# Kernel optimization log

Hardware: AMD Instinct MI355X
Metric: run time of the kernel (lower is better)

Reference implementation:

```python
import jax, jax.numpy as jnp
import numpy as np

# CODABlocks (codomain attention) with per_channel_attention=True:
# token_codimension = head_codimension = 1, scale = 2, n_modes = [32, 32],
# mixer_modes = [16, 16], temperature = 1.0, instance_norm (affine) everywhere.
N_HEADS = 16
TEMPERATURE = 1.0
EPS = 1e-5

def _gelu(z):
    return jax.nn.gelu(z, approximate=False)  # matches torch F.gelu default (erf)

def instance_norm(x, g, b):
    # x: (B, C, H, W); normalize over spatial dims per (sample, channel), affine.
    mu = jnp.mean(x, axis=(-2, -1), keepdims=True)
    var = jnp.var(x, axis=(-2, -1), keepdims=True)
    return (x - mu) * jax.lax.rsqrt(var + EPS) * g[:, None, None] + b[:, None, None]

def conv1x1(x, w, b):
    return jnp.einsum('bihw,io->bohw', x, w) + b[None, :, None, None]

def fourier_resample(x, out_shape):
    # FFT-based spatial resampling (mode truncation / zero-pad), norm='forward'.
    if tuple(x.shape[-2:]) == tuple(out_shape):
        return x
    Ho, Wo = out_shape
    xft = jnp.fft.rfftn(x, axes=(-2, -1), norm='forward')
    out = jnp.zeros(x.shape[:-2] + (Ho, Wo // 2 + 1), dtype=xft.dtype)
    hk = min(x.shape[-2], Ho) // 2
    wk = min(xft.shape[-1], Wo // 2 + 1)
    out = out.at[..., :hk, :wk].set(xft[..., :hk, :wk])
    out = out.at[..., -hk:, :wk].set(xft[..., -hk:, :wk])
    return jnp.fft.irfftn(out, s=out_shape, axes=(-2, -1), norm='forward')

def spectral_conv(x, w, out_shape):
    # Truncated-mode spectral convolution (dense weights, equiv. to tucker rank=1.0).
    # w: (Cin, Cout, 2*mh, mw, 2) -> complex weight on kept Fourier modes.
    wc = w[..., 0] + 1j * w[..., 1]
    mh = wc.shape[2] // 2
    mw = wc.shape[3]
    Ho, Wo = out_shape
    xft = jnp.fft.rfftn(x, axes=(-2, -1), norm='forward')   # (B, Cin, H, W//2+1)
    top = jnp.einsum('bihw,iohw->bohw', xft[:, :, :mh, :mw], wc[:, :, :mh])
    bot = jnp.einsum('bihw,iohw->bohw', xft[:, :, -mh:, :mw], wc[:, :, mh:])
    out_ft = jnp.zeros((x.shape[0], wc.shape[1], Ho, Wo // 2 + 1), dtype=xft.dtype)
    out_ft = out_ft.at[:, :, :mh, :mw].set(top)
    out_ft = out_ft.at[:, :, -mh:, :mw].set(bot)
    return jnp.fft.irfftn(out_ft, s=out_shape, axes=(-2, -1), norm='forward')

def fno_layer(x, spec_w, skip_w, skip_b, out_shape, norm=None, act=None):
    # One FNOBlocks layer: spectral conv + (resampled) linear skip, optional norm/act.
    xs = fourier_resample(conv1x1(x, skip_w, skip_b), out_shape)
    xf = spectral_conv(x, spec_w, out_shape)
    if norm is not None:
        xf = instance_norm(xf, *norm)
    y = xf + xs
    return act(y) if act is not None else y

def codano_forward(x, key_w, key_skip_w, key_skip_b, query_w, query_skip_w, query_skip_b, value_w, value_skip_w, value_skip_b, proj_w, proj_skip_w, proj_skip_b, norm1_g, norm1_b, attn_norm_g, attn_norm_b, norm2_g, norm2_b, mixer_w1, mixer_skip_w1, mixer_skip_b1, mixer_norm_g1, mixer_norm_b1, mixer_w2, mixer_skip_w2, mixer_skip_b2, mixer_norm_g2, mixer_norm_b2, mixer_out_g, mixer_out_b):
    b, t, H, W = x.shape   # token codim d = 1 -> channel dim == number of tokens
    tokens = x.reshape(b * t, 1, H, W)
    tokens_norm = instance_norm(tokens, norm1_g, norm1_b)
    Hs, Ws = H // 2, W // 2   # K, Q downsampled by scale = 2
    k = fno_layer(tokens_norm, key_w, key_skip_w, key_skip_b, (Hs, Ws))
    q = fno_layer(tokens_norm, query_w, query_skip_w, query_skip_b, (Hs, Ws))
    v = fno_layer(tokens_norm, value_w, value_skip_w, value_skip_b, (H, W))

    def heads_flat(z):
        hh, ww = z.shape[-2:]
        # (b*t, n_heads*d, h, w) -> (b, heads, t, d*h*w), d = 1
        return z.reshape(b, t, N_HEADS, hh * ww).transpose(0, 2, 1, 3)

    kf, qf, vf = heads_flat(k), heads_flat(q), heads_flat(v)
    scale = jnp.sqrt(jnp.asarray(kf.shape[-1], jnp.float32)) * TEMPERATURE
    dprod = jax.nn.softmax(jnp.einsum('bhtd,bhsd->bhts', qf, kf) / scale, axis=-1)
    attn = jnp.einsum('bhts,bhsd->bhtd', dprod, vf)      # (b, heads, t, H*W)
    attn = attn.transpose(0, 2, 1, 3).reshape(b * t, N_HEADS, H, W)
    # multi-head projection back to token codimension (n_heads -> 1)
    attn = fno_layer(attn, proj_w, proj_skip_w, proj_skip_b, (H, W))
    attn = instance_norm(attn + tokens, attn_norm_g, attn_norm_b)
    # permutation-equivariant mixer: 2 FNO layers shared across all tokens
    m = instance_norm(attn, norm2_g, norm2_b)
    m = fno_layer(m, mixer_w1, mixer_skip_w1, mixer_skip_b1, (H, W), norm=(mixer_norm_g1, mixer_norm_b1), act=_gelu)
    m = fno_layer(m, mixer_w2, mixer_skip_w2, mixer_skip_b2, (H, W), norm=(mixer_norm_g2, mixer_norm_b2))
    out = instance_norm(m, mixer_out_g, mixer_out_b) + attn
    return out.reshape(b, t, H, W)

def setup_inputs():
    key = jax.random.key(0)
    ks = list(jax.random.split(key, 32))
    f32 = jnp.float32
    def W_(k, shape, s=0.02):
        return (s * jax.random.normal(k, shape)).astype(f32)
    B, T, H, Wd = 4, 32, 128, 128
    mh_s, mw_s = 16, 9    # mixer_modes [16,16]: 2*(16//2) rows, 16//2+1 rfft cols
    mh_f, mw_f = 32, 17   # n_modes [32,32]
    return {
        'x': jax.random.normal(ks[0], (B, T, H, Wd), dtype=f32),
        'key_w': W_(ks[1], (1, N_HEADS, mh_s, mw_s, 2)),
        'key_skip_w': W_(ks[2], (1, N_HEADS), 0.5),
        'key_skip_b': W_(ks[3], (N_HEADS,)),
        'query_w': W_(ks[4], (1, N_HEADS, mh_s, mw_s, 2)),
        'query_skip_w': W_(ks[5], (1, N_HEADS), 0.5),
        'query_skip_b': W_(ks[6], (N_HEADS,)),
        'value_w': W_(ks[7], (1, N_HEADS, mh_s, mw_s, 2)),
        'value_skip_w': W_(ks[8], (1, N_HEADS), 0.5),
        'value_skip_b': W_(ks[9], (N_HEADS,)),
        'proj_w': W_(ks[10], (N_HEADS, 1, mh_f, mw_f, 2)),
        'proj_skip_w': W_(ks[11], (N_HEADS, 1), 0.25),
        'proj_skip_b': W_(ks[12], (1,)),
        'norm1_g': jnp.ones((1,), f32), 'norm1_b': jnp.zeros((1,), f32),
        'attn_norm_g': jnp.ones((1,), f32), 'attn_norm_b': jnp.zeros((1,), f32),
        'norm2_g': jnp.ones((1,), f32), 'norm2_b': jnp.zeros((1,), f32),
        'mixer_w1': W_(ks[13], (1, 1, mh_f, mw_f, 2)),
        'mixer_skip_w1': W_(ks[14], (1, 1), 0.5),
        'mixer_skip_b1': W_(ks[15], (1,)),
        'mixer_norm_g1': jnp.ones((1,), f32), 'mixer_norm_b1': jnp.zeros((1,), f32),
        'mixer_w2': W_(ks[16], (1, 1, mh_f, mw_f, 2)),
        'mixer_skip_w2': W_(ks[17], (1, 1), 0.5),
        'mixer_skip_b2': W_(ks[18], (1,)),
        'mixer_norm_g2': jnp.ones((1,), f32), 'mixer_norm_b2': jnp.zeros((1,), f32),
        'mixer_out_g': jnp.ones((1,), f32), 'mixer_out_b': jnp.zeros((1,), f32),
    }

def reference(x, key_w, key_skip_w, key_skip_b, query_w, query_skip_w, query_skip_b, value_w, value_skip_w, value_skip_b, proj_w, proj_skip_w, proj_skip_b, norm1_g, norm1_b, attn_norm_g, attn_norm_b, norm2_g, norm2_b, mixer_w1, mixer_skip_w1, mixer_skip_b1, mixer_norm_g1, mixer_norm_b1, mixer_w2, mixer_skip_w2, mixer_skip_b2, mixer_norm_g2, mixer_norm_b2, mixer_out_g, mixer_out_b):
    return codano_forward(x, key_w, key_skip_w, key_skip_b, query_w, query_skip_w, query_skip_b, value_w, value_skip_w, value_skip_b, proj_w, proj_skip_w, proj_skip_b, norm1_g, norm1_b, attn_norm_g, attn_norm_b, norm2_g, norm2_b, mixer_w1, mixer_skip_w1, mixer_skip_b1, mixer_norm_g1, mixer_norm_b1, mixer_w2, mixer_skip_w2, mixer_skip_b2, mixer_norm_g2, mixer_norm_b2, mixer_out_g, mixer_out_b)
```

## Files before the change

### kernel.cpp

```cpp
#include <hip/hip_runtime.h>
#include <cmath>

#define PI_F 3.14159265358979323846f
#define NTOK 128
#define NPIX 16384
#define NHEADS 16

__device__ __forceinline__ void block_reduce2(float& a, float& b){
  __shared__ float sa[4], sb[4];
  __syncthreads();
  for (int o=32;o>0;o>>=1){ a += __shfl_down(a,o); b += __shfl_down(b,o); }
  int w = threadIdx.x>>6, l = threadIdx.x&63;
  if (l==0){ sa[w]=a; sb[w]=b; }
  __syncthreads();
  a = sa[0]+sa[1]+sa[2]+sa[3];
  b = sb[0]+sb[1]+sb[2]+sb[3];
}

__device__ __forceinline__ float block_reduce1(float a){
  __shared__ float sa[4];
  __syncthreads();
  for (int o=32;o>0;o>>=1) a += __shfl_down(a,o);
  int w = threadIdx.x>>6, l = threadIdx.x&63;
  if (l==0) sa[w]=a;
  __syncthreads();
  return sa[0]+sa[1]+sa[2]+sa[3];
}

__device__ __forceinline__ float br1k(float a, float* scr){
  __syncthreads();
  for (int o=32;o>0;o>>=1) a += __shfl_down(a,o);
  int w=threadIdx.x>>6, l=threadIdx.x&63;
  if (l==0) scr[w]=a;
  __syncthreads();
  if (threadIdx.x<64){
    float v=(threadIdx.x<16)? scr[threadIdx.x] : 0.f;
    for (int o=8;o>0;o>>=1) v += __shfl_down(v,o);
    if (threadIdx.x==0) scr[16]=v;
  }
  __syncthreads();
  return scr[16];
}

__device__ __forceinline__ float gelu_f(float y){
  return 0.5f*y*(1.f + erff(y*0.70710678118f));
}

__device__ __forceinline__ void affine_from(const float* __restrict__ ps, float g, float bb, int t,
                                            float& a, float& b0){
  float sum=0.f,sq=0.f;
  #pragma unroll
  for (int s=0;s<8;s++){ const float* p=ps+((size_t)t*8+s)*2; sum+=p[0]; sq+=p[1]; }
  const float iN=1.f/NPIX;
  float mu=sum*iN, var=sq*iN-mu*mu;
  a=rsqrtf(var+1e-5f)*g;
  b0=bb-mu*a;
}
__device__ __forceinline__ void scalA_from(const float* __restrict__ psA, float ag, float n2g, int t,
                                           float& muZ, float& aA, float& a0){
  float sum=0.f,sq=0.f;
  #pragma unroll
  for (int s=0;s<16;s++){ const float* p=psA+((size_t)t*16+s)*2; sum+=p[0]; sq+=p[1]; }
  const float iN=1.f/NPIX;
  muZ=sum*iN; float var=sq*iN-muZ*muZ;
  float inv=rsqrtf(var+1e-5f);
  aA=inv*ag;
  float var2=aA*aA*var;
  a0=aA*rsqrtf(var2+1e-5f)*n2g;
}

__global__ __launch_bounds__(256) void k_scol(const float* __restrict__ x,
                        float* __restrict__ A, float* __restrict__ pstat){
  __shared__ float rows[2048];
  __shared__ float S1[2592];
  __shared__ float tw[256];
  int bx=blockIdx.x;
  int base = bx*16;
  float sum=0.f, sq=0.f;
  for (int i=threadIdx.x;i<2048;i+=256){
    float v = x[(size_t)base*128 + i];
    rows[i]=v; sum+=v; sq+=v*v;
  }
  for (int p=threadIdx.x;p<128;p+=256){ float sn,cs; sincosf(-(2.f*PI_F/128.f)*(float)p,&sn,&cs); tw[p*2]=cs; tw[p*2+1]=sn; }
  __syncthreads();
  for (int e=threadIdx.x;e<1280;e+=256){
    int r=e/80, q=e%80, w0=q/5, k=q%5;
    const float* y=rows+r*128+w0;
    float re=0.f, im=0.f;
    #pragma unroll
    for (int w1=0;w1<8;w1++){
      int p=(16*k*w1)&127;
      float v=y[w1*16];
      re+=v*tw[p*2]; im+=v*tw[p*2+1];
    }
    float* o=S1+r*162+q*2; o[0]=re; o[1]=im;
  }
  __syncthreads();
  for (int e=threadIdx.x;e<528;e+=256){
    int r=e/33, c=e%33;
    int m=c&7; int ks=m; float sg=1.f;
    if (m>4){ ks=8-m; sg=-1.f; }
    const float* Sp=S1+r*162+ks*2;
    float re=0.f, im=0.f;
    #pragma unroll
    for (int w0=0;w0<16;w0++){
      int p=(c*w0)&127;
      float cr=tw[p*2], ci=tw[p*2+1];
      float sr=Sp[w0*10], si=sg*Sp[w0*10+1];
      re += sr*cr - si*ci;
      im += sr*ci + si*cr;
    }
    float* o=A+((size_t)(base+r)*33+c)*2; o[0]=re; o[1]=im;
  }
  block_reduce2(sum,sq);
  if (threadIdx.x==0){ float* o=pstat+(size_t)bx*2; o[0]=sum; o[1]=sq; }
}

__global__ __launch_bounds__(256) void k_rowfft64(const float* __restrict__ A,
                          const float* __restrict__ pstat0,
                          const float* __restrict__ n1g, const float* __restrict__ n1b,
                          float* __restrict__ X64, float* __restrict__ X64h){
  int s=blockIdx.x, cg2=blockIdx.y;
  int c0=cg2*11;
  __shared__ float a[128*11*2];
  __shared__ float S1[11*290];
  __shared__ float S[64][11][2];
  __shared__ float tw[128][2];
  for (int i=threadIdx.x;i<128*22;i+=256){
    int r=i/22, q=i%22;
    a[(r*11+(q>>1))*2+(q&1)] = A[((size_t)(s*128+r)*33 + c0)*2 + q];
  }
  for (int p=threadIdx.x;p<128;p+=256){ float sn,cs; sincosf(-(2.f*PI_F/128.f)*(float)p,&sn,&cs); tw[p][0]=cs; tw[p][1]=sn; }
  float af,b0; affine_from(pstat0, n1g[0], n1b[0], s, af, b0);
  __syncthreads();
  for (int e=threadIdx.x;e<1408;e+=256){
    int cl=e>>7, q=e&127, h0=q>>3, k=q&7;
    float re=0.f, im=0.f;
    #pragma unroll
    for (int h1=0;h1<8;h1++){
      int p=(16*k*h1)&127;
      float cr=tw[p][0], ci=tw[p][1];
      const float* ap=a+((h0+16*h1)*11+cl)*2;
      float ar=ap[0], ai=ap[1];
      re += ar*cr - ai*ci;
      im += ar*ci + ai*cr;
    }
    float* o=S1+cl*290+h0*18+k*2; o[0]=re; o[1]=im;
  }
  __syncthreads();
  const float sc=1.f/16384.f;
  for (int e=threadIdx.x;e<64*11;e+=256){
    int i2=e/11, cl=e%11;
    int r=(i2<32)? i2 : i2+64;
    int k=r&7;
    const float* Sp=S1+cl*290+k*2;
    float re=0.f, im=0.f;
    #pragma unroll
    for (int h0=0;h0<16;h0++){
      int p=(r*h0)&127;
      float cr=tw[p][0], ci=tw[p][1];
      float sr=Sp[h0*18], si=Sp[h0*18+1];
      re += sr*cr - si*ci;
      im += sr*ci + si*cr;
    }
    float vr = af*re*sc, vi = af*im*sc;
    if (r==0 && (c0+cl)==0) vr += b0;
    S[i2][cl][0]=vr; S[i2][cl][1]=vi;
  }
  __syncthreads();
  for (int e=threadIdx.x;e<64*11;e+=256){
    int r=e/11, cl=e%11; int c=c0+cl;
    float vr=S[r][cl][0], vi=S[r][cl][1];
    float* o=X64+((size_t)s*(64*33)+r*33+c)*2; o[0]=vr; o[1]=vi;
    float hr=vr, hi=vi;
    if (c==0 || c==32){
      int pr=(64-r)&63;
      hr=0.5f*(vr+S[pr][cl][0]);
      hi=0.5f*(vi-S[pr][cl][1]);
    }
    float* oh=X64h+((size_t)s*(64*33)+r*33+c)*2; oh[0]=hr; oh[1]=hi;
  }
}

__global__ __launch_bounds__(256) void k_UeZYw(const float* __restrict__ X64, const float* __restrict__ X64h,
    const float* __restrict__ qw, const float* __restrict__ qsw,
    const float* __restrict__ kw, const float* __restrict__ ksw,
    const float* __restrict__ value_w, const float* __restrict__ vsw, const float* __restrict__ vsb,
    const float* __restrict__ proj_w, const float* __restrict__ psw,
    float* __restrict__ Zq, float* __restrict__ Zk, float* __restrict__ Yw,
    float* __restrict__ Ue){
  __shared__ float sh[4224];
  int bx=blockIdx.x;
  if (bx<2048){
    int t=bx>>4, h=bx&15;
    float* Xs = sh;
    float2* xh0 = (float2*)(sh+1092);
    for (int e=threadIdx.x;e<544;e+=256){
      int j=e/17, c=e%17;
      int i2=(j<16)? j : (j+32);
      const float* xp = X64 + ((size_t)t*(64*33) + i2*33 + c)*2;
      Xs[e*2]=xp[0]; Xs[e*2+1]=xp[1];
    }
    if (threadIdx.x<17){
      int j=threadIdx.x;
      int r=(j<=8)? j : j+47;
      const float* hp = X64h + ((size_t)t*(64*33) + r*33)*2;
      xh0[j]=make_float2(hp[0],hp[1]);
    }
    __syncthreads();
    float aq=qsw[h], ak=ksw[h];
    for (int e=threadIdx.x;e<306;e+=256){
      int side=e/153, m=e%153;
      int j=m/9, c=m%9;
      int jj=(j<=8)? j : j+15;
      const float* W = side? kw : qw;
      float a = side? ak : aq;
      float prx=0.f, pry=0.f;
      if (j!=8){
        int jw=(j<8)? j : j-1;
        const float* wp = W + ((size_t)(h*16+jw)*9 + c)*2;
        float xrr=Xs[(jj*17+c)*2], xri=Xs[(jj*17+c)*2+1];
        prx = wp[0]*xrr - wp[1]*xri;
        pry = wp[0]*xri + wp[1]*xrr;
      }
      float Vx=prx, Vy=pry;
      if (c==0){
        int jp = (j==0)? 0 : 17-j;
        float ppx=0.f, ppy=0.f;
        if (jp!=8){
          int jw2=(jp<8)? jp : jp-1;
          const float* wp2 = W + ((size_t)(h*16+jw2)*9)*2;
          int jj2=(jp<=8)? jp : jp+15;
          float x2r=Xs[(jj2*17)*2], x2i=Xs[(jj2*17)*2+1];
          ppx = wp2[0]*x2r - wp2[1]*x2i;
          ppy = wp2[0]*x2i + wp2[1]*x2r;
        }
        Vx = 0.5f*(prx + ppx);
        Vy = 0.5f*(pry - ppy);
      }
      float xmr, xmi;
      if (c==0){ xmr=xh0[j].x; xmi=xh0[j].y; }
      else { xmr=Xs[(jj*17+c)*2]; xmi=Xs[(jj*17+c)*2+1]; }
      float zr = a*xmr + Vx;
      float zi = a*xmi + Vy;
      float wf = (side && c!=0)? 2.f : 1.f;
      float* dst = (side? Zk : Zq) + ((size_t)(t*16+h))*306 + m*2;
      dst[0]=wf*zr; dst[1]=wf*zi;
    }
    int b=t>>5, s=t&31;
    float vw_=vsw[h], vb=vsb[h], pw=psw[h];
    size_t obase = ((size_t)(b*16+h)*32 + s)*1088;
    for (int e=threadIdx.x;e<544;e+=256){
      int j=e/17, c=e%17;
      float xr=Xs[e*2], xi=Xs[e*2+1];
      float wvr=0.f,wvi=0.f;
      if (c<=8 && (j<8||j>=24)){
        int jw=(j<8)? j : (j-16);
        const float* wv = value_w + ((size_t)(h*16+jw)*9 + c)*2;
        wvr=wv[0]; wvi=wv[1];
      }
      float Mr=xr*wvr-xi*wvi, Mi=xr*wvi+xi*wvr;
      float Mhr=Mr, Mhi=Mi;
      if (c==0){
        float Pr2=0.f,Pi2=0.f;
        int jp2=(j==0)?0:((j==16)?-1:32-j);
        if (jp2>=0 && (jp2<8||jp2>=24)){
          int jw2=(jp2<8)? jp2 : (jp2-16);
          const float* wv2=value_w+((size_t)(h*16+jw2)*9)*2;
          float pxr=Xs[(jp2*17)*2], pxi=Xs[(jp2*17)*2+1];
          Pr2=pxr*wv2[0]-pxi*wv2[1];
          Pi2=pxr*wv2[1]+pxi*wv2[0];
        }
        Mhr=0.5f*(Mr+Pr2); Mhi=0.5f*(Mi-Pi2);
      }
      float Yr=vw_*xr+Mhr+((e==0)? vb:0.f);
      float Yi=vw_*xi+Mhi;
      const float* pc=proj_w+((size_t)(h*32+j)*17+c)*2;
      float pr=pc[0], pi=pc[1];
      float* o=Yw+obase+e*2;
      o[0]=pr*Yr-pi*Yi+pw*Mr;
      o[1]=pr*Yi+pi*Yr+pw*Mi;
    }
  } else {
    int u=bx-2048;
    int b=u>>8, rem=u&255, t=rem>>3, sg=rem&7;
    float2* xt=(float2*)sh;
    const float2* src = (const float2*)(X64h + ((size_t)(b*32+t))*4224);
    for (int m=threadIdx.x;m<2112;m+=256){
      int r=m/33, c=m%33;
      bool excl = (c<=8) && (r<=8 || r>=56);
      float w = excl? 0.f : ((c==0||c==32)? 1.f : 2.f);
      float2 v = src[m];
      xt[m]=make_float2(v.x*w, v.y*w);
    }
    __syncthreads();
    float acc[4]={0.f,0.f,0.f,0.f};
    const float2* s0=(const float2*)(X64h + ((size_t)(b*32+sg*4))*4224);
    for (int m=threadIdx.x;m<2112;m+=256){
      float2 a2=xt[m];
      #pragma unroll
      for (int j=0;j<4;j++){
        float2 b2=s0[(size_t)j*2112+m];
        acc[j]+=a2.x*b2.x+a2.y*b2.y;
      }
    }
    for (int j=0;j<4;j++){
      float r=block_reduce1(acc[j]);
      if (threadIdx.x==0) Ue[((size_t)(b*32+t))*32 + sg*4+j]=r;
    }
  }
}

__global__ __launch_bounds__(256) void k_scores2(const float* __restrict__ Zq, const float* __restrict__ Zk,
                          const float* __restrict__ Ue,
                          const float* __restrict__ qsw, const float* __restrict__ qsb,
                          const float* __restrict__ ksw, const float* __restrict__ ksb,
                          float* __restrict__ P){
  int b=blockIdx.x, h=blockIdx.y, tz=blockIdx.z;
  __shared__ float2 zq[16][154];
  __shared__ float2 zk[16][154];
  __shared__ float Pl[16][33];
  for (int i=threadIdx.x;i<16*153;i+=256){
    int t=i/153, m=i%153;
    zq[t][m]=((const float2*)(Zq + ((size_t)((b*32+tz*16+t)*16+h))*306))[m];
  }
  float aq=qsw[h], ak=ksw[h], bq=qsb[h], bk=ksb[h];
  float aqak=aq*ak;
  int tl=threadIdx.x>>4, sl=threadIdx.x&15;
  for (int ch=0; ch<2; ch++){
    __syncthreads();
    for (int i=threadIdx.x;i<16*153;i+=256){
      int s=i/153, m=i%153;
      zk[s][m]=((const float2*)(Zk + ((size_t)((b*32+ch*16+s)*16+h))*306))[m];
    }
    __syncthreads();
    float acc=0.f;
    for (int m=0;m<153;m++){
      float2 a2=zq[tl][m], c2=zk[sl][m];
      acc += a2.x*c2.x + a2.y*c2.y;
    }
    int s=ch*16+sl;
    float G = aqak*Ue[((size_t)(b*32+tz*16+tl))*32+s] + acc;
    Pl[tl][s] = 64.f*(G + bk*zq[tl][0].x + bq*zk[sl][0].x + bq*bk);
  }
  __syncthreads();
  if (threadIdx.x<16){
    int tt=threadIdx.x;
    float mx=-INFINITY;
    for (int s=0;s<32;s++) mx=fmaxf(mx,Pl[tt][s]);
    float e[32]; float sum=0.f;
    for (int s=0;s<32;s++){ e[s]=expf(Pl[tt][s]-mx); sum+=e[s]; }
    float inv=1.f/sum;
    size_t base=((size_t)(b*16+h)*32+tz*16+tt)*32;
    for (int s=0;s<32;s++) P[base+s]=e[s]*inv;
  }
}

__global__ __launch_bounds__(256) void k_SfSk(const float* __restrict__ x, const float* __restrict__ P,
        const float* __restrict__ Yw,
        const float* __restrict__ pw, const float* __restrict__ vw,
        const float* __restrict__ pstat0, const float* __restrict__ n1g, const float* __restrict__ n1b,
        float* __restrict__ Sfp, float* __restrict__ sk){
  __shared__ float sh[4096];
  int bx=blockIdx.x;
  if (bx<272){
    int b=bx/68, rem=bx%68, ec=rem/4, g=rem%4;
    int e0=ec*64, hs0=g*128;
    float (*Pl)[32] = (float(*)[32])sh;
    for (int i=threadIdx.x;i<128*32;i+=256){
      int hsl=i>>5, t=i&31;
      int hs=hs0+hsl, h=hs>>5, s=hs&31;
      Pl[hsl][t]=P[(((size_t)(b*16+h)*32)+t)*32+s];
    }
    __syncthreads();
    int el=threadIdx.x&63, tg=threadIdx.x>>6;
    float acc[8];
    #pragma unroll
    for (int j=0;j<8;j++) acc[j]=0.f;
    const float* Yb = Yw + ((size_t)b*512 + hs0)*1088 + e0 + el;
    #pragma unroll 4
    for (int hsl=0;hsl<128;hsl++){
      float y = Yb[(size_t)hsl*1088];
      #pragma unroll
      for (int j=0;j<8;j++) acc[j] += Pl[hsl][tg*8+j]*y;
    }
    #pragma unroll
    for (int j=0;j<8;j++){
      int t=tg*8+j;
      Sfp[((size_t)(b*32+t)*4+g)*1088 + e0 + el] = acc[j];
    }
  } else {
    int u=bx-272;
    int b=u>>6, rem=u&63, ch=rem>>1, tt=rem&1;
    int pxb=ch*512;
    float* Rs = sh;
    float* cbs = sh+512;
    float* as2 = sh+528;
    float* b0s = sh+560;
    if (threadIdx.x<32){
      float a,b0; affine_from(pstat0, n1g[0], n1b[0], b*32+threadIdx.x, a, b0);
      as2[threadIdx.x]=a; b0s[threadIdx.x]=b0;
    }
    __syncthreads();
    for (int rr=threadIdx.x; rr<512; rr+=256){
      int tl=rr>>5, s=rr&31;
      int t=tt*16+tl;
      float acc=0.f;
      for (int h=0;h<16;h++)
        acc += pw[h]*vw[h]*P[(((size_t)(b*16+h)*32)+t)*32+s];
      Rs[tl*32+s]=acc*as2[s];
      float cb=acc*b0s[s];
      for (int o=16;o>0;o>>=1) cb+=__shfl_down(cb,o,32);
      if (s==0) cbs[tl]=cb;
    }
    __syncthreads();
    float a0[16], a1[16];
    #pragma unroll
    for (int t=0;t<16;t++){ a0[t]=0.f; a1[t]=0.f; }
    for (int s=0;s<32;s++){
      const float* xp = x + ((size_t)(b*32+s))*NPIX + pxb;
      float v0=xp[threadIdx.x], v1=xp[threadIdx.x+256];
      #pragma unroll
      for (int t=0;t<16;t++){ float r=Rs[t*32+s]; a0[t]+=r*v0; a1[t]+=r*v1; }
    }
    #pragma unroll
    for (int t=0;t<16;t++){
      int gt=tt*16+t;
      float cb=cbs[t];
      float* op = sk + ((size_t)(b*32+gt))*NPIX + pxb;
      op[threadIdx.x]=a0[t]+cb; op[threadIdx.x+256]=a1[t]+cb;
    }
  }
}

__global__ __launch_bounds__(256) void k_f0sp(const float* __restrict__ Sfp,
        const float* __restrict__ sk, const float* __restrict__ x,
        const float* __restrict__ P, const float* __restrict__ X64,
        const float* __restrict__ pstat0,
        const float* __restrict__ n1g, const float* __restrict__ n1b,
        const float* __restrict__ pw, const float* __restrict__ vw,
        const float* __restrict__ psw, const float* __restrict__ vsb, const float* __restrict__ psb,
        float* __restrict__ zf, float* __restrict__ pstatA, float* __restrict__ sp){
  __shared__ float sh[1616];
  int bx=blockIdx.x;
  if (bx<2048){
    int bt=bx>>4, slab=bx&15;
    float* Ss=sh; float* T=sh+1088; float* tw=sh+1360;
    for (int i=threadIdx.x;i<1088;i+=256){
      const float* sp4 = Sfp + (size_t)bt*4352 + i;
      Ss[i] = sp4[0]+sp4[1088]+sp4[2176]+sp4[3264];
    }
    for (int q=threadIdx.x;q<128;q+=256){ float sn,cs; sincosf((2.f*PI_F/128.f)*(float)q,&sn,&cs); tw[q*2]=cs; tw[q*2+1]=sn; }
    __syncthreads();
    int h0 = slab*8;
    for (int e=threadIdx.x;e<136;e+=256){
      int hl=e/17, c=e%17; int h=h0+hl;
      float re=0.f, im=0.f;
      for (int j=0;j<32;j++){
        int r=(j<16)? j : (j+96);
        int p=(r*h)&127;
        float cs=tw[p*2], sn=tw[p*2+1];
        float ar=Ss[(j*17+c)*2], ai=Ss[(j*17+c)*2+1];
        re += ar*cs - ai*sn;
        im += ar*sn + ai*cs;
      }
      T[e*2]=re; T[e*2+1]=im;
    }
    __syncthreads();
    size_t base = (size_t)bt*NPIX + h0*128;
    float Cb = psb[0];
    for (int hh=0;hh<16;hh++) Cb += psw[hh]*vsb[hh];
    int w=threadIdx.x&127, hl0=threadIdx.x>>7;
    float cw[16], swt[16];
    #pragma unroll
    for (int c=0;c<16;c++){ int p=((c+1)*w)&127; cw[c]=tw[p*2]; swt[c]=tw[p*2+1]; }
    float sum=0.f, sq=0.f;
    #pragma unroll
    for (int pp=0;pp<4;pp++){
      int hl=hl0+2*pp;
      const float2* Th=(const float2*)(T+hl*34);
      float v=Th[0].x;
      #pragma unroll
      for (int c=0;c<16;c++){ float2 th=Th[c+1]; v += 2.f*(th.x*cw[c] - th.y*swt[c]); }
      int pos=hl*128+w;
      float val = v + sk[base+pos] + x[base+pos] + Cb;
      zf[base+pos]=val; sum+=val; sq+=val*val;
    }
    block_reduce2(sum,sq);
    if (threadIdx.x==0){ float* o=pstatA+((size_t)bt*16+slab)*2; o[0]=sum; o[1]=sq; }
  } else {
    int u=bx-2048;
    int bt=u>>1, ec=u&1; int b=bt>>5, t=bt&31;
    float* Sfl=sh; float* Rs=sh+1088;
    if (threadIdx.x<32){
      int s=threadIdx.x; float acc=0.f;
      for (int h=0;h<16;h++)
        acc += pw[h]*vw[h]*P[(((size_t)(b*16+h)*32)+t)*32+s];
      Rs[s]=acc;
    }
    for (int i=threadIdx.x;i<1088;i+=256){
      const float* sp4 = Sfp + (size_t)bt*4352 + i;
      Sfl[i]=sp4[0]+sp4[1088]+sp4[2176]+sp4[3264];
    }
    __syncthreads();
    float a_t,b0_t; affine_from(pstat0,n1g[0],n1b[0],bt,a_t,b0_t);
    float Cb=psb[0];
    for (int h=0;h<16;h++) Cb+=psw[h]*vsb[h];
    float inva=1.f/a_t;
    int e1=ec*272, e2=e1+272;
    for (int e=e1+threadIdx.x;e<e2;e+=256){
      int j=e/17, c=e%17;
      float sr=Sfl[e*2], si=Sfl[e*2+1];
      if (c==0){
        if (j==0){ si=0.f; }
        else if (j==16){ sr*=0.5f; si*=0.5f; }
        else { int jp=32-j; sr=0.5f*(sr+Sfl[jp*34]); si=0.5f*(si-Sfl[jp*34+1]); }
      }
      int i2=(j<16)? j : (j+32);
      float re=0.f, im=0.f;
      const float* xb = X64 + ((size_t)(b*32)*(64*33) + i2*33 + c)*2;
      for (int s=0;s<32;s++){
        const float* xp = xb + (size_t)s*(64*33)*2;
        float r=Rs[s];
        re += r*xp[0]; im += r*xp[1];
      }
      const float* xt = X64 + ((size_t)bt*(64*33) + i2*33 + c)*2;
      re += inva*xt[0]; im += inva*xt[1];
      float zr=sr+re, zi=si+im;
      if (e==0) zr += Cb - b0_t*inva;
      sp[((size_t)bt*544+e)*2]=zr; sp[((size_t)bt*544+e)*2+1]=zi;
    }
  }
}

__global__ __launch_bounds__(1024,1) void k_tail(const float* __restrict__ sp,
    const float* __restrict__ wm1, const float* __restrict__ wm2,
    const float* __restrict__ zf, const float* __restrict__ pstatA,
    const float* __restrict__ ag, const float* __restrict__ n2g, const float* __restrict__ n2b,
    const float* __restrict__ mng1, const float* __restrict__ mnb1,
    const float* __restrict__ msw1, const float* __restrict__ msb1,
    const float* __restrict__ mng2, const float* __restrict__ mnb2,
    const float* __restrict__ msw2, const float* __restrict__ msb2,
    const float* __restrict__ ab, const float* __restrict__ outg, const float* __restrict__ outb,
    float* __restrict__ out){
  __shared__ float T1A[4352];
  __shared__ float T2[4352];
  __shared__ float m1s[16384];
  __shared__ float S1[2592];
  __shared__ float spb[1088];
  __shared__ float tw[256];
  __shared__ float red[20];
  int bt=blockIdx.x, tid=threadIdx.x;
  float muZ,aA,a0;
  scalA_from(pstatA, ag[0], n2g[0], bt, muZ, aA, a0);
  float b2=n2b[0];
  float d0=b2 - muZ*a0;
  for (int e=tid;e<544;e+=1024){
    float xr=a0*sp[((size_t)bt*544+e)*2] + ((e==0)? d0:0.f);
    float xi=a0*sp[((size_t)bt*544+e)*2+1];
    float wr=wm1[e*2], wi=wm1[e*2+1];
    spb[e*2]=xr*wr-xi*wi; spb[e*2+1]=xr*wi+xi*wr;
  }
  for (int p=tid;p<128;p+=1024){ float sn,cs; sincosf((2.f*PI_F/128.f)*(float)p,&sn,&cs); tw[p*2]=cs; tw[p*2+1]=sn; }
  __syncthreads();
  for (int e=tid;e<2176;e+=1024){
    int h=e/17, c=e%17;
    float re=0.f, im=0.f;
    for (int j=0;j<32;j++){
      int r=(j<16)? j : (j+96);
      int p=(r*h)&127;
      float cs=tw[p*2], sn=tw[p*2+1];
      float ar=spb[(j*17+c)*2], ai=spb[(j*17+c)*2+1];
      re += ar*cs - ai*sn;
      im += ar*sn + ai*cs;
    }
    T1A[e*2]=re; T1A[e*2+1]=im;
  }
  __syncthreads();
  int w=tid&127, h0=tid>>7;
  float cw[16], swt[16];
  #pragma unroll
  for (int c=0;c<16;c++){ int p=((c+1)*w)&127; cw[c]=tw[p*2]; swt[c]=tw[p*2+1]; }
  float sum1=0.f, sq1=0.f;
  for (int p=0;p<16;p++){
    int h=h0+8*p;
    const float* Th=T1A+h*34;
    float v=Th[0];
    #pragma unroll
    for (int c=0;c<16;c++){ v += 2.f*(Th[(c+1)*2]*cw[c] - Th[(c+1)*2+1]*swt[c]); }
    m1s[h*128+w]=v; sum1+=v; sq1+=v*v;
  }
  float S1s=br1k(sum1,red);
  float Q1s=br1k(sq1,red);
  const float iN=1.f/16384.f;
  float mu1=S1s*iN;
  float var1=Q1s*iN - mu1*mu1;
  float c1=rsqrtf(var1+1e-5f)*mng1[0];
  float nb1=mnb1[0], sw1=msw1[0], sb1=msb1[0];
  size_t base=(size_t)bt*NPIX;
  for (int p=0;p<16;p++){
    int h=h0+8*p;
    int idx=h*128+w;
    size_t gi=base+idx;
    float m0v=(zf[gi]-muZ)*a0+b2;
    float y=(m1s[idx]-mu1)*c1+nb1 + m0v*sw1 + sb1;
    m1s[idx]=gelu_f(y);
  }
  __syncthreads();
  for (int chn=0; chn<8; chn++){
    int grow=chn*16;
    for (int e=tid;e<1280;e+=1024){
      int r=e/80, q=e%80, w0=q/5, k=q%5;
      const float* y=m1s+(grow+r)*128+w0;
      float re=0.f, im=0.f;
      #pragma unroll
      for (int w1=0;w1<8;w1++){
        int p=(16*k*w1)&127;
        float v=y[w1*16];
        re += v*tw[p*2];
        im -= v*tw[p*2+1];
      }
      float* o=S1+r*162+q*2; o[0]=re; o[1]=im;
    }
    __syncthreads();
    for (int e=tid;e<272;e+=1024){
      int r=e/17, c=e%17;
      int m=c&7, ks=m; float sg=1.f;
      if (m>4){ ks=8-m; sg=-1.f; }
      const float* Sp=S1+r*162+ks*2;
      float re=0.f, im=0.f;
      #pragma unroll
      for (int w0=0;w0<16;w0++){
        int p=(c*w0)&127;
        float cs=tw[p*2], sn=tw[p*2+1];
        float sr=Sp[w0*10], si=sg*Sp[w0*10+1];
        re += sr*cs + si*sn;
        im += -sr*sn + si*cs;
      }
      T1A[((grow+r)*17+c)*2]=re; T1A[((grow+r)*17+c)*2+1]=im;
    }
    __syncthreads();
  }
  const float sc=1.f/16384.f;
  for (int e=tid;e<544;e+=1024){
    int j=e/17, c=e%17;
    int r=(j<16)? j : (j+96);
    float re=0.f, im=0.f;
    for (int h=0;h<128;h++){
      int p=(r*h)&127;
      float cs=tw[p*2], sn=tw[p*2+1];
      float ar=T1A[(h*17+c)*2], ai=T1A[(h*17+c)*2+1];
      re += ar*cs + ai*sn;
      im += -ar*sn + ai*cs;
    }
    spb[e*2]=re*sc; spb[e*2+1]=im*sc;
  }
  __syncthreads();
  for (int e=tid;e<544;e+=1024){
    float xr=spb[e*2], xi=spb[e*2+1];
    float wr=wm2[e*2], wi=wm2[e*2+1];
    spb[e*2]=xr*wr-xi*wi; spb[e*2+1]=xr*wi+xi*wr;
  }
  __syncthreads();
  for (int e=tid;e<2176;e+=1024){
    int h=e/17, c=e%17;
    float re=0.f, im=0.f;
    for (int j=0;j<32;j++){
      int r=(j<16)? j : (j+96);
      int p=(r*h)&127;
      float cs=tw[p*2], sn=tw[p*2+1];
      float ar=spb[(j*17+c)*2], ai=spb[(j*17+c)*2+1];
      re += ar*cs - ai*sn;
      im += ar*sn + ai*cs;
    }
    T2[e*2]=re; T2[e*2+1]=im;
  }
  __syncthreads();
  float s_f=0.f, s_fsq=0.f, s_m=0.f, s_msq=0.f, s_x=0.f;
  for (int p=0;p<16;p++){
    int h=h0+8*p;
    const float* Th=T2+h*34;
    float v=Th[0];
    #pragma unroll
    for (int c=0;c<16;c++){ v += 2.f*(Th[(c+1)*2]*cw[c] - Th[(c+1)*2+1]*swt[c]); }
    float m1v=m1s[h*128+w];
    s_f+=v; s_fsq+=v*v; s_m+=m1v; s_msq+=m1v*m1v; s_x+=v*m1v;
  }
  float Sf=br1k(s_f,red);
  float Sfsq=br1k(s_fsq,red);
  float Sm=br1k(s_m,red);
  float Smsq=br1k(s_msq,red);
  float Sx=br1k(s_x,red);
  float mu2f=Sf*iN;
  float var2=Sfsq*iN - mu2f*mu2f;
  float c2=rsqrtf(var2+1e-5f)*mng2[0];
  float Em1=Sm*iN, Em1sq=Smsq*iN, Exm=Sx*iN;
  float K=mnb2[0]+msb2[0], sw2=msw2[0];
  float Em2=K+sw2*Em1;
  float Em2sq=c2*c2*var2 + sw2*sw2*Em1sq + K*K + 2.f*c2*sw2*(Exm-mu2f*Em1) + 2.f*K*sw2*Em1;
  float mu3=Em2;
  float c3=rsqrtf(Em2sq-Em2*Em2+1e-5f)*outg[0];
  float b1=ab[0], nb2=mnb2[0], sb2=msb2[0], bo=outb[0];
  for (int p=0;p<16;p++){
    int h=h0+8*p;
    const float* Th=T2+h*34;
    float v=Th[0];
    #pragma unroll
    for (int c=0;c<16;c++){ v += 2.f*(Th[(c+1)*2]*cw[c] - Th[(c+1)*2+1]*swt[c]); }
    size_t gi=base+(size_t)h*128+w;
    float a2v=(zf[gi]-muZ)*aA+b1;
    float m1v=m1s[h*128+w];
    float m2v=(v-mu2f)*c2+nb2 + m1v*sw2 + sb2;
    out[gi]=(m2v-mu3)*c3+bo+a2v;
  }
}

extern "C" void kernel_launch(void* const* d_in, const int* in_sizes, int n_in,
                              void* d_out, int out_size, void* d_ws, size_t ws_size,
                              hipStream_t stream){
  const float* x        = (const float*)d_in[0];
  const float* key_w    = (const float*)d_in[1];
  const float* key_sw   = (const float*)d_in[2];
  const float* key_sb   = (const float*)d_in[3];
  const float* query_w  = (const float*)d_in[4];
  const float* query_sw = (const float*)d_in[5];
  const float* query_sb = (const float*)d_in[6];
  const float* value_w  = (const float*)d_in[7];
  const float* value_sw = (const float*)d_in[8];
  const float* value_sb = (const float*)d_in[9];
  const float* proj_w   = (const float*)d_in[10];
  const float* proj_sw  = (const float*)d_in[11];
  const float* proj_sb  = (const float*)d_in[12];
  const float* norm1_g  = (const float*)d_in[13];
  const float* norm1_b  = (const float*)d_in[14];
  const float* attn_g   = (const float*)d_in[15];
  const float* attn_b   = (const float*)d_in[16];
  const float* norm2_g  = (const float*)d_in[17];
  const float* norm2_b  = (const float*)d_in[18];
  const float* mw1      = (const float*)d_in[19];
  const float* msw1     = (const float*)d_in[20];
  const float* msb1     = (const float*)d_in[21];
  const float* mng1     = (const float*)d_in[22];
  const float* mnb1     = (const float*)d_in[23];
  const float* mw2      = (const float*)d_in[24];
  const float* msw2     = (const float*)d_in[25];
  const float* msb2     = (const float*)d_in[26];
  const float* mng2     = (const float*)d_in[27];
  const float* mnb2     = (const float*)d_in[28];
  const float* outg     = (const float*)d_in[29];
  const float* outb     = (const float*)d_in[30];
  float* out = (float*)d_out;
  float* ws  = (float*)d_ws;

  size_t off=0;
  float* A   = ws + off; off += (size_t)128*128*33*2;
  float* X64 = ws + off; off += (size_t)128*64*33*2;
  float* X64h= ws + off; off += (size_t)128*64*33*2;
  float* Zq  = ws + off; off += (size_t)128*16*306;
  float* Zk  = ws + off; off += (size_t)128*16*306;
  float* Ue  = ws + off; off += (size_t)4*32*32;
  float* P   = ws + off; off += (size_t)4*16*32*32;
  float* Yw  = ws + off; off += (size_t)2048*1088;
  float* Sfp = ws + off; off += (size_t)128*4*1088;
  float* sk  = ws + off; off += (size_t)128*16384;
  float* zf  = ws + off; off += (size_t)128*16384;
  float* sp  = ws + off; off += (size_t)128*544*2;
  float* pstat0 = ws + off; off += (size_t)128*8*2;
  float* pstatA = ws + off; off += (size_t)128*16*2;

  k_scol<<<1024,256,0,stream>>>(x, A, pstat0);
  k_rowfft64<<<dim3(128,3),256,0,stream>>>(A, pstat0, norm1_g, norm1_b, X64, X64h);
  k_UeZYw<<<3072,256,0,stream>>>(X64, X64h, query_w, query_sw, key_w, key_sw,
      value_w, value_sw, value_sb, proj_w, proj_sw, Zq, Zk, Yw, Ue);
  k_scores2<<<dim3(4,16,2),256,0,stream>>>(Zq, Zk, Ue, query_sw, query_sb, key_sw, key_sb, P);
  k_SfSk<<<528,256,0,stream>>>(x, P, Yw, proj_sw, value_sw, pstat0, norm1_g, norm1_b, Sfp, sk);
  k_f0sp<<<2304,256,0,stream>>>(Sfp, sk, x, P, X64, pstat0, norm1_g, norm1_b,
      proj_sw, value_sw, proj_sw, value_sb, proj_sb, zf, pstatA, sp);
  k_tail<<<128,1024,0,stream>>>(sp, mw1, mw2, zf, pstatA,
      attn_g, norm2_g, norm2_b, mng1, mnb1, msw1, msb1,
      mng2, mnb2, msw2, msb2, attn_b, outg, outb, out);
}
```

Measured before the change: 277.8 us.

## Split tail kernel across two blocks per sample with inter-block flag sync

The fused tail kernel now runs two 1024-thread blocks per sample, each handling half the spatial rows. The blocks exchange partial norm statistics and partial spectral sums through global workspace, synchronising with atomic flags and spin-waits. Shared memory per block shrinks, and the second-stage spatial values are cached in shared memory rather than recomputed. This doubles parallelism (256 blocks instead of 128) at the cost of three cross-block handshakes and a memset, and it depends on both blocks of a pair being co-resident to avoid deadlock.

New measurement: 500.6 us. +80.2%, slower.

```diff
diff --git a/kernel.cpp b/kernel.cpp
--- a/kernel.cpp
+++ b/kernel.cpp
@@ -533,7 +533,7 @@
   }
 }
 
-__global__ __launch_bounds__(1024,1) void k_tail(const float* __restrict__ sp,
+__global__ __launch_bounds__(1024,1) void k_tail2(const float* __restrict__ sp,
     const float* __restrict__ wm1, const float* __restrict__ wm2,
     const float* __restrict__ zf, const float* __restrict__ pstatA,
     const float* __restrict__ ag, const float* __restrict__ n2g, const float* __restrict__ n2b,
@@ -542,29 +542,31 @@
     const float* __restrict__ mng2, const float* __restrict__ mnb2,
     const float* __restrict__ msw2, const float* __restrict__ msb2,
     const float* __restrict__ ab, const float* __restrict__ outg, const float* __restrict__ outb,
+    float* __restrict__ xst, float* __restrict__ xsp, float* __restrict__ xmo,
+    unsigned* __restrict__ flg,
     float* __restrict__ out){
-  __shared__ float T1A[4352];
-  __shared__ float T2[4352];
-  __shared__ float m1s[16384];
-  __shared__ float S1[2592];
-  __shared__ float spb[1088];
+  __shared__ float m1s[8192];
+  __shared__ float fd2s[8192];
+  __shared__ float Tbuf[2176];
+  __shared__ float arena[2592];
   __shared__ float tw[256];
   __shared__ float red[20];
-  int bt=blockIdx.x, tid=threadIdx.x;
+  int blk=blockIdx.x, bt=blk>>1, half=blk&1, tid=threadIdx.x;
+  int hbase=half*64;
+  float* spb=arena; float* S1=arena;
   float muZ,aA,a0;
   scalA_from(pstatA, ag[0], n2g[0], bt, muZ, aA, a0);
-  float b2=n2b[0];
-  float d0=b2 - muZ*a0;
+  float b2=n2b[0], d0=b2-muZ*a0;
   for (int e=tid;e<544;e+=1024){
     float xr=a0*sp[((size_t)bt*544+e)*2] + ((e==0)? d0:0.f);
     float xi=a0*sp[((size_t)bt*544+e)*2+1];
     float wr=wm1[e*2], wi=wm1[e*2+1];
     spb[e*2]=xr*wr-xi*wi; spb[e*2+1]=xr*wi+xi*wr;
   }
-  for (int p=tid;p<128;p+=1024){ float sn,cs; sincosf((2.f*PI_F/128.f)*(float)p,&sn,&cs); tw[p*2]=cs; tw[p*2+1]=sn; }
-  __syncthreads();
-  for (int e=tid;e<2176;e+=1024){
-    int h=e/17, c=e%17;
+  if (tid<128){ float sn,cs; sincosf((2.f*PI_F/128.f)*(float)tid,&sn,&cs); tw[tid*2]=cs; tw[tid*2+1]=sn; }
+  __syncthreads();
+  for (int e=tid;e<1088;e+=1024){
+    int lh=e/17, c=e%17; int h=hbase+lh;
     float re=0.f, im=0.f;
     for (int j=0;j<32;j++){
       int r=(j<16)? j : (j+96);
@@ -574,7 +576,7 @@
       re += ar*cs - ai*sn;
       im += ar*sn + ai*cs;
     }
-    T1A[e*2]=re; T1A[e*2+1]=im;
+    Tbuf[e*2]=re; Tbuf[e*2+1]=im;
   }
   __syncthreads();
   int w=tid&127, h0=tid>>7;
@@ -582,32 +584,42 @@
   #pragma unroll
   for (int c=0;c<16;c++){ int p=((c+1)*w)&127; cw[c]=tw[p*2]; swt[c]=tw[p*2+1]; }
   float sum1=0.f, sq1=0.f;
-  for (int p=0;p<16;p++){
-    int h=h0+8*p;
-    const float* Th=T1A+h*34;
+  #pragma unroll
+  for (int p=0;p<8;p++){
+    int lh=h0+8*p;
+    const float* Th=Tbuf+lh*34;
     float v=Th[0];
     #pragma unroll
     for (int c=0;c<16;c++){ v += 2.f*(Th[(c+1)*2]*cw[c] - Th[(c+1)*2+1]*swt[c]); }
-    m1s[h*128+w]=v; sum1+=v; sq1+=v*v;
-  }
-  float S1s=br1k(sum1,red);
-  float Q1s=br1k(sq1,red);
+    m1s[lh*128+w]=v; sum1+=v; sq1+=v*v;
+  }
+  float Sh=br1k(sum1,red);
+  float Qh=br1k(sq1,red);
+  if (tid==0){
+    xst[(size_t)bt*4+half*2]=Sh; xst[(size_t)bt*4+half*2+1]=Qh;
+    __threadfence();
+    atomicAdd(&flg[bt],1u);
+    while (__hip_atomic_load(&flg[bt],__ATOMIC_RELAXED,__HIP_MEMORY_SCOPE_AGENT)<2u)
+      __builtin_amdgcn_s_sleep(1);
+  }
+  __syncthreads();
+  __threadfence();
   const float iN=1.f/16384.f;
-  float mu1=S1s*iN;
-  float var1=Q1s*iN - mu1*mu1;
-  float c1=rsqrtf(var1+1e-5f)*mng1[0];
+  float mu1=(xst[(size_t)bt*4]+xst[(size_t)bt*4+2])*iN;
+  float q1=(xst[(size_t)bt*4+1]+xst[(size_t)bt*4+3])*iN;
+  float c1=rsqrtf(q1-mu1*mu1+1e-5f)*mng1[0];
   float nb1=mnb1[0], sw1=msw1[0], sb1=msb1[0];
   size_t base=(size_t)bt*NPIX;
-  for (int p=0;p<16;p++){
-    int h=h0+8*p;
-    int idx=h*128+w;
-    size_t gi=base+idx;
+  #pragma unroll
+  for (int p=0;p<8;p++){
+    int lh=h0+8*p; int idx=lh*128+w;
+    size_t gi=base+(size_t)(hbase+lh)*128+w;
     float m0v=(zf[gi]-muZ)*a0+b2;
     float y=(m1s[idx]-mu1)*c1+nb1 + m0v*sw1 + sb1;
     m1s[idx]=gelu_f(y);
   }
   __syncthreads();
-  for (int chn=0; chn<8; chn++){
+  for (int chn=0; chn<4; chn++){
     int grow=chn*16;
     for (int e=tid;e<1280;e+=1024){
       int r=e/80, q=e%80, w0=q/5, k=q%5;
@@ -637,33 +649,43 @@
         re += sr*cs + si*sn;
         im += -sr*sn + si*cs;
       }
-      T1A[((grow+r)*17+c)*2]=re; T1A[((grow+r)*17+c)*2+1]=im;
-    }
-    __syncthreads();
-  }
+      Tbuf[((grow+r)*17+c)*2]=re; Tbuf[((grow+r)*17+c)*2+1]=im;
+    }
+    __syncthreads();
+  }
+  if (tid<544){
+    int j=tid/17, c=tid%17;
+    int r=(j<16)? j : (j+96);
+    float re=0.f, im=0.f;
+    for (int lh=0;lh<64;lh++){
+      int p=(r*(hbase+lh))&127;
+      float cs=tw[p*2], sn=tw[p*2+1];
+      float ar=Tbuf[(lh*17+c)*2], ai=Tbuf[(lh*17+c)*2+1];
+      re += ar*cs + ai*sn;
+      im += -ar*sn + ai*cs;
+    }
+    xsp[(size_t)blk*1088+tid*2]=re;
+    xsp[(size_t)blk*1088+tid*2+1]=im;
+  }
+  __threadfence();
+  __syncthreads();
+  if (tid==0){
+    atomicAdd(&flg[128+bt],1u);
+    while (__hip_atomic_load(&flg[128+bt],__ATOMIC_RELAXED,__HIP_MEMORY_SCOPE_AGENT)<2u)
+      __builtin_amdgcn_s_sleep(1);
+  }
+  __syncthreads();
+  __threadfence();
   const float sc=1.f/16384.f;
   for (int e=tid;e<544;e+=1024){
-    int j=e/17, c=e%17;
-    int r=(j<16)? j : (j+96);
-    float re=0.f, im=0.f;
-    for (int h=0;h<128;h++){
-      int p=(r*h)&127;
-      float cs=tw[p*2], sn=tw[p*2+1];
-      float ar=T1A[(h*17+c)*2], ai=T1A[(h*17+c)*2+1];
-      re += ar*cs + ai*sn;
-      im += -ar*sn + ai*cs;
-    }
-    spb[e*2]=re*sc; spb[e*2+1]=im*sc;
-  }
-  __syncthreads();
-  for (int e=tid;e<544;e+=1024){
-    float xr=spb[e*2], xi=spb[e*2+1];
+    float xr=(xsp[(size_t)(bt*2)*1088+e*2]  +xsp[(size_t)(bt*2+1)*1088+e*2])*sc;
+    float xi=(xsp[(size_t)(bt*2)*1088+e*2+1]+xsp[(size_t)(bt*2+1)*1088+e*2+1])*sc;
     float wr=wm2[e*2], wi=wm2[e*2+1];
     spb[e*2]=xr*wr-xi*wi; spb[e*2+1]=xr*wi+xi*wr;
   }
   __syncthreads();
-  for (int e=tid;e<2176;e+=1024){
-    int h=e/17, c=e%17;
+  for (int e=tid;e<1088;e+=1024){
+    int lh=e/17, c=e%17; int h=hbase+lh;
     float re=0.f, im=0.f;
     for (int j=0;j<32;j++){
       int r=(j<16)? j : (j+96);
@@ -673,17 +695,19 @@
       re += ar*cs - ai*sn;
       im += ar*sn + ai*cs;
     }
-    T2[e*2]=re; T2[e*2+1]=im;
+    Tbuf[e*2]=re; Tbuf[e*2+1]=im;
   }
   __syncthreads();
   float s_f=0.f, s_fsq=0.f, s_m=0.f, s_msq=0.f, s_x=0.f;
-  for (int p=0;p<16;p++){
-    int h=h0+8*p;
-    const float* Th=T2+h*34;
+  #pragma unroll
+  for (int p=0;p<8;p++){
+    int lh=h0+8*p; int idx=lh*128+w;
+    const float* Th=Tbuf+lh*34;
     float v=Th[0];
     #pragma unroll
     for (int c=0;c<16;c++){ v += 2.f*(Th[(c+1)*2]*cw[c] - Th[(c+1)*2+1]*swt[c]); }
-    float m1v=m1s[h*128+w];
+    float m1v=m1s[idx];
+    fd2s[idx]=v;
     s_f+=v; s_fsq+=v*v; s_m+=m1v; s_msq+=m1v*m1v; s_x+=v*m1v;
   }
   float Sf=br1k(s_f,red);
@@ -691,26 +715,33 @@
   float Sm=br1k(s_m,red);
   float Smsq=br1k(s_msq,red);
   float Sx=br1k(s_x,red);
-  float mu2f=Sf*iN;
-  float var2=Sfsq*iN - mu2f*mu2f;
+  if (tid==0){
+    float* o=xmo+(size_t)bt*16+half*8;
+    o[0]=Sf; o[1]=Sfsq; o[2]=Sm; o[3]=Smsq; o[4]=Sx;
+    __threadfence();
+    atomicAdd(&flg[256+bt],1u);
+    while (__hip_atomic_load(&flg[256+bt],__ATOMIC_RELAXED,__HIP_MEMORY_SCOPE_AGENT)<2u)
+      __builtin_amdgcn_s_sleep(1);
+  }
+  __syncthreads();
+  __threadfence();
+  const float* mo=xmo+(size_t)bt*16;
+  float mu2f=(mo[0]+mo[8])*iN;
+  float var2=(mo[1]+mo[9])*iN - mu2f*mu2f;
   float c2=rsqrtf(var2+1e-5f)*mng2[0];
-  float Em1=Sm*iN, Em1sq=Smsq*iN, Exm=Sx*iN;
+  float Em1=(mo[2]+mo[10])*iN, Em1sq=(mo[3]+mo[11])*iN, Exm=(mo[4]+mo[12])*iN;
   float K=mnb2[0]+msb2[0], sw2=msw2[0];
   float Em2=K+sw2*Em1;
   float Em2sq=c2*c2*var2 + sw2*sw2*Em1sq + K*K + 2.f*c2*sw2*(Exm-mu2f*Em1) + 2.f*K*sw2*Em1;
   float mu3=Em2;
   float c3=rsqrtf(Em2sq-Em2*Em2+1e-5f)*outg[0];
   float b1=ab[0], nb2=mnb2[0], sb2=msb2[0], bo=outb[0];
-  for (int p=0;p<16;p++){
-    int h=h0+8*p;
-    const float* Th=T2+h*34;
-    float v=Th[0];
-    #pragma unroll
-    for (int c=0;c<16;c++){ v += 2.f*(Th[(c+1)*2]*cw[c] - Th[(c+1)*2+1]*swt[c]); }
-    size_t gi=base+(size_t)h*128+w;
+  #pragma unroll
+  for (int p=0;p<8;p++){
+    int lh=h0+8*p; int idx=lh*128+w;
+    size_t gi=base+(size_t)(hbase+lh)*128+w;
     float a2v=(zf[gi]-muZ)*aA+b1;
-    float m1v=m1s[h*128+w];
-    float m2v=(v-mu2f)*c2+nb2 + m1v*sw2 + sb2;
+    float m2v=(fd2s[idx]-mu2f)*c2+nb2 + m1s[idx]*sw2 + sb2;
     out[gi]=(m2v-mu3)*c3+bo+a2v;
   }
 }
@@ -767,7 +798,12 @@
   float* sp  = ws + off; off += (size_t)128*544*2;
   float* pstat0 = ws + off; off += (size_t)128*8*2;
   float* pstatA = ws + off; off += (size_t)128*16*2;
-
+  float* xst = ws + off; off += (size_t)128*4;
+  float* xsp = ws + off; off += (size_t)256*1088;
+  float* xmo = ws + off; off += (size_t)128*16;
+  unsigned* flg = (unsigned*)(ws + off); off += 384;
+
+  hipMemsetAsync(flg, 0, 384*sizeof(unsigned), stream);
   k_scol<<<1024,256,0,stream>>>(x, A, pstat0);
   k_rowfft64<<<dim3(128,3),256,0,stream>>>(A, pstat0, norm1_g, norm1_b, X64, X64h);
   k_UeZYw<<<3072,256,0,stream>>>(X64, X64h, query_w, query_sw, key_w, key_sw,
@@ -776,7 +812,8 @@
   k_SfSk<<<528,256,0,stream>>>(x, P, Yw, proj_sw, value_sw, pstat0, norm1_g, norm1_b, Sfp, sk);
   k_f0sp<<<2304,256,0,stream>>>(Sfp, sk, x, P, X64, pstat0, norm1_g, norm1_b,
       proj_sw, value_sw, proj_sw, value_sb, proj_sb, zf, pstatA, sp);
-  k_tail<<<128,1024,0,stream>>>(sp, mw1, mw2, zf, pstatA,
+  k_tail2<<<256,1024,0,stream>>>(sp, mw1, mw2, zf, pstatA,
       attn_g, norm2_g, norm2_b, mng1, mnb1, msw1, msb1,
-      mng2, mnb2, msw2, msb2, attn_b, outg, outb, out);
-}
+      mng2, mnb2, msw2, msb2, attn_b, outg, outb,
+      xst, xsp, xmo, flg, out);
+}
```
